# Optimization experiments

Measured on AMD Instinct MI355X. Metric: run time of the kernel, lower is better.

Reference implementation:

```python
import jax, jax.numpy as jnp
import numpy as np

B, H, W = 8, 1024, 1280
EPS = 1e-7
MIN_DEPTH, MAX_DEPTH = 10.0, 255.0


def _constants(batch, view_to_syn='left'):
    trans = np.array([-4.14339018, -0.0238197036, -0.00190685259], np.float32)
    K_u = np.array([1035.30811, 0.0, 596.955017, 0.0, 1035.08765, 520.410034, 0.0, 0.0, 1.0], np.float32).reshape(3, 3)
    K_u[0, :] /= 1280.0
    K_u[1, :] /= 1024.0
    K_u4 = np.zeros((4, 4), np.float32); K_u4[:3, :3] = K_u; K_u4[3, 3] = 1.0
    K_d = np.array([1035.17419, 0.0, 688.361877, 0.0, 1034.979, 521.070801, 0.0, 0.0, 1.0], np.float32).reshape(3, 3)
    K_d[0, :] /= 1280.0
    K_d[1, :] /= 1024.0
    K_d4 = np.zeros((4, 4), np.float32); K_d4[:3, :3] = K_d; K_d4[3, 3] = 1.0
    if view_to_syn == 'right':
        src, tgt, t = K_u4, K_d4, trans
    else:
        src, tgt, t = K_d4, K_u4, -trans
    source_K = jnp.asarray(np.tile(src[None], (batch, 1, 1)))
    target_K = jnp.asarray(np.tile(tgt[None], (batch, 1, 1)))
    trans_vec = jnp.asarray(np.tile(t[None], (batch, 1)))
    return source_K, target_K, trans_vec


def setup_inputs() -> dict:
    key = jax.random.key(0)
    k1, k2 = jax.random.split(key)
    img = jax.random.normal(k1, (B, 3, H, W), jnp.float32)
    pred_disp = jax.random.uniform(k2, (B, 1, H, W), jnp.float32)
    source_K, target_K, trans_vec = _constants(B, 'left')
    return {"img": img, "pred_disp": pred_disp, "source_K": source_K,
            "target_K": target_K, "trans_vec": trans_vec}


def _grid_sample_border(img, grid):
    """Bilinear grid_sample, padding_mode='border', align_corners=False (torch default).
    img: [B,C,H,W], grid: [B,H,W,2] in [-1,1] (x,y). Returns [B,C,H,W]."""
    b, c, h, w = img.shape
    x = (grid[..., 0] + 1.0) * w * 0.5 - 0.5  # [B,H,W]
    y = (grid[..., 1] + 1.0) * h * 0.5 - 0.5
    x0f = jnp.floor(x); y0f = jnp.floor(y)
    wx = (x - x0f)[:, None]  # [B,1,H,W]
    wy = (y - y0f)[:, None]
    x0 = jnp.clip(x0f.astype(jnp.int32), 0, w - 1)
    x1 = jnp.clip(x0f.astype(jnp.int32) + 1, 0, w - 1)
    y0 = jnp.clip(y0f.astype(jnp.int32), 0, h - 1)
    y1 = jnp.clip(y0f.astype(jnp.int32) + 1, 0, h - 1)
    gather = jax.vmap(lambda im, yi, xi: im[:, yi, xi])  # -> [B,C,H,W]
    i00 = gather(img, y0, x0)
    i01 = gather(img, y0, x1)
    i10 = gather(img, y1, x0)
    i11 = gather(img, y1, x1)
    return (i00 * (1 - wx) * (1 - wy) + i01 * wx * (1 - wy)
            + i10 * (1 - wx) * wy + i11 * wx * wy)


def reference(img, pred_disp, source_K, target_K, trans_vec):
    b, _, h, w = img.shape
    # disp -> depth
    min_disp, max_disp = 1.0 / MAX_DEPTH, 1.0 / MIN_DEPTH
    scaled_disp = min_disp + (max_disp - min_disp) * pred_disp
    depth = 1.0 / scaled_disp  # [B,1,H,W]
    # homogeneous pixel grid [3, H*W]
    xs, ys = jnp.meshgrid(jnp.arange(w, dtype=jnp.float32),
                          jnp.arange(h, dtype=jnp.float32), indexing='xy')
    pix = jnp.stack([xs.reshape(-1), ys.reshape(-1), jnp.ones(h * w, jnp.float32)], 0)
    # backproject
    inv_K = jnp.linalg.inv(source_K)[:, :3, :3]  # [B,3,3]
    cam = jnp.einsum('bij,jn->bin', inv_K, pix) * depth.reshape(b, 1, -1)  # [B,3,HW]
    cam4 = jnp.concatenate([cam, jnp.ones((b, 1, h * w), cam.dtype)], axis=1)  # [B,4,HW]
    # extrinsic: R = I, so T @ R = translation matrix
    T = jnp.tile(jnp.eye(4, dtype=img.dtype)[None], (b, 1, 1)).at[:, :3, 3].set(trans_vec.reshape(b, 3))
    P = jnp.matmul(target_K, T)[:, :3, :]  # [B,3,4]
    cp = jnp.matmul(P, cam4)  # [B,3,HW]
    pc = cp[:, :2] / (cp[:, 2:3] + EPS)  # [B,2,HW]
    pc = pc.reshape(b, 2, h, w).transpose(0, 2, 3, 1)  # [B,H,W,2]
    scale = jnp.array([w - 1, h - 1], dtype=pc.dtype)
    grid = (pc / scale - 0.5) * 2.0
    return _grid_sample_border(img, grid)
```

## Files before the change

### kernel.cpp

```cpp
#include <hip/hip_runtime.h>

#define BB 8
#define HH 1024
#define WW 1280
#define HW (HH * WW)
#define EPSF 1e-7f

#define TH 16
#define TCOLS 264
#define SROWS 18
#define CPR 66
#define CCH (SROWS * CPR)
#define CPT 5
#define STF (CPT * 256 * 4)

#define GAS __attribute__((address_space(1)))
#define LAS __attribute__((address_space(3)))

typedef float f4 __attribute__((ext_vector_type(4)));

__device__ __forceinline__ float fast_rcp(float x) {
    float r = __builtin_amdgcn_rcpf(x);
    r = r * __builtin_fmaf(-x, r, 2.0f);
    return r;
}

__global__ void precompute_consts(
    const float* __restrict__ srcK, const float* __restrict__ tgtK,
    const float* __restrict__ trans, float* __restrict__ cb)
{
    const int b = threadIdx.x;
    if (b >= BB) return;
    const float* sK = srcK + b * 16;
    const float* tK = tgtK + b * 16;
    const float* tv = trans + b * 3;

    const float fsx = sK[0], csx = sK[2];
    const float fsy = sK[5], csy = sK[6];
    const float ftx = tK[0], ctx = tK[2];
    const float fty = tK[5], cty = tK[6];
    const float t0 = tv[0], t1 = tv[1], t2 = tv[2];

    const float Sx = (float)WW / (float)(WW - 1);
    const float Sy = (float)HH / (float)(HH - 1);
    const float rfsx = 1.0f / fsx;
    const float rfsy = 1.0f / fsy;
    float* c = cb + b * 8;
    c[0] = ftx * rfsx * Sx;
    c[1] = __builtin_fmaf(-ftx * csx, rfsx, ctx) * Sx;
    c[2] = (ftx * t0 + ctx * t2) * Sx;
    c[3] = fty * rfsy * Sy;
    c[4] = __builtin_fmaf(-fty * csy, rfsy, cty) * Sy;
    c[5] = (fty * t1 + cty * t2) * Sy;
    c[6] = t2 + EPSF;
    c[7] = 0.0f;
}

__global__ __launch_bounds__(256, 4) void synth_view_kernel(
    const float* __restrict__ img, const float* __restrict__ disp,
    const float* __restrict__ cbuf, float* __restrict__ out)
{
    __shared__ __align__(16) float st[STF];

    const int tid = threadIdx.x;
    const int wid = blockIdx.x;
    const int r   = wid & 7;
    int q = wid >> 3;
    const int tyl = q & 7;  q >>= 3;
    const int xb  = q % 5;
    const int b   = q / 5;
    const int y0  = (r * 8 + tyl) * TH;
    const int x0  = xb * 256;
    const int x   = x0 + tid;

    const float* imb = img + (size_t)b * 3 * HW;

    const float* db = disp + (size_t)b * HW + (size_t)y0 * WW + x;
    float dsp[TH];
#pragma unroll
    for (int j = 0; j < TH; ++j)
        dsp[j] = __builtin_nontemporal_load(db + j * WW);

    int goff[CPT];
#pragma unroll
    for (int i = 0; i < CPT; ++i) {
        const int qq = i * 256 + tid;
        const int qc = min(qq, CCH - 1);
        const int ri = qc / CPR;
        const int k  = qc - ri * CPR;
        const int row = min(max(y0 - 1 + ri, 0), HH - 1);
        const int col = min(max(x0 - 4 + 4 * k, 0), WW - 4);
        goff[i] = row * WW + col;
    }

#pragma unroll
    for (int i = 0; i < CPT; ++i)
        __builtin_amdgcn_global_load_lds(
            (const GAS unsigned int*)(const void*)(imb + goff[i]),
            (LAS unsigned int*)(void*)&st[(i * 256 + tid) * 4], 16, 0, 0);

    const float* cb = cbuf + b * 8;
    const float A00 = cb[0], A02 = cb[1], C0 = cb[2];
    const float A11 = cb[3], A12 = cb[4], C1 = cb[5];
    const float t2e = cb[6];

    const float mind = 1.0f / 255.0f;
    const float rng  = 0.1f - mind;
    const float axc  = __builtin_fmaf(A00, (float)x, A02);

    int   lb[TH]; float wxa[TH], wya[TH];
#pragma unroll
    for (int j = 0; j < TH; ++j) {
        const int y = y0 + j;
        const float sd  = __builtin_fmaf(dsp[j], rng, mind);
        const float rrz = fast_rcp(__builtin_fmaf(t2e, sd, 1.0f));
        const float ayc = __builtin_fmaf(A11, (float)y, A12);
        const float sx  = __builtin_fmaf(__builtin_fmaf(C0, sd, axc), rrz, -0.5f);
        const float sy  = __builtin_fmaf(__builtin_fmaf(C1, sd, ayc), rrz, -0.5f);

        const int ixc = min(max((int)floorf(sx), 0), WW - 2);
        const int iyc = min(max((int)floorf(sy), 0), HH - 2);
        wxa[j] = fminf(fmaxf(sx - (float)ixc, 0.0f), 1.0f);
        wya[j] = fminf(fmaxf(sy - (float)iyc, 0.0f), 1.0f);
        const int wcol = min(max(ixc - x0 + 4, 0), TCOLS - 2);
        const int wrow = min(max(iyc - y0 + 1, 0), SROWS - 2);
        lb[j] = (wrow * TCOLS + wcol) * 4;
    }

    float* outb = out + (size_t)b * 3 * HW + (size_t)y0 * WW + x;

    for (int c = 0; c < 3; ++c) {
        if (c > 0) {
            __syncthreads();
#pragma unroll
            for (int i = 0; i < CPT; ++i)
                __builtin_amdgcn_global_load_lds(
                    (const GAS unsigned int*)(const void*)(imb + (size_t)c * HW + goff[i]),
                    (LAS unsigned int*)(void*)&st[(i * 256 + tid) * 4], 16, 0, 0);
        }
        __syncthreads();

        float* oc = outb + (size_t)c * HW;
#pragma unroll
        for (int j = 0; j < TH; ++j) {
            const float* p = (const float*)((const char*)st + lb[j]);
            const float wx = wxa[j], wy = wya[j];
            const float wxm = 1.0f - wx, wym = 1.0f - wy;
            float acc =          p[0]         * (wxm * wym);
            acc = __builtin_fmaf(p[1],         wx * wym, acc);
            acc = __builtin_fmaf(p[TCOLS],     wxm * wy, acc);
            acc = __builtin_fmaf(p[TCOLS + 1], wx * wy,  acc);
            __builtin_nontemporal_store(acc, oc + j * WW);
        }
    }
}

extern "C" void kernel_launch(void* const* d_in, const int* in_sizes, int n_in,
                              void* d_out, int out_size, void* d_ws, size_t ws_size,
                              hipStream_t stream) {
    const float* img   = (const float*)d_in[0];
    const float* disp  = (const float*)d_in[1];
    const float* srcK  = (const float*)d_in[2];
    const float* tgtK  = (const float*)d_in[3];
    const float* trans = (const float*)d_in[4];
    float* out = (float*)d_out;
    float* cb  = (float*)d_ws;

    precompute_consts<<<dim3(1), dim3(64), 0, stream>>>(srcK, tgtK, trans, cb);

    dim3 block(256, 1, 1);
    dim3 grid(5 * 64 * BB, 1, 1);
    synth_view_kernel<<<grid, block, 0, stream>>>(img, disp, cb, out);
}
```

Before: 253.9 us.

## Split channels across separate blocks instead of looping per block

Each block now handles one color channel, so the grid is three times larger and the serial per-channel loop with its extra barriers and LDS reloads is gone. The disparity load switches from nontemporal to a normal cached load, since each disparity tile is now read by three blocks. This adds parallelism and removes the intra-block channel serialization, at the cost of recomputing the projection coordinates three times and reading disparity three times.

New measurement: 256.1 us. About the same (+0.9%).

```diff
diff --git a/kernel.cpp b/kernel.cpp
--- a/kernel.cpp
+++ b/kernel.cpp
@@ -16,8 +16,6 @@
 
 #define GAS __attribute__((address_space(1)))
 #define LAS __attribute__((address_space(3)))
-
-typedef float f4 __attribute__((ext_vector_type(4)));
 
 __device__ __forceinline__ float fast_rcp(float x) {
     float r = __builtin_amdgcn_rcpf(x);
@@ -64,8 +62,10 @@
 
     const int tid = threadIdx.x;
     const int wid = blockIdx.x;
-    const int r   = wid & 7;
-    int q = wid >> 3;
+    const int c   = wid / 2560;
+    const int t   = wid - c * 2560;
+    const int r   = t & 7;
+    int q = t >> 3;
     const int tyl = q & 7;  q >>= 3;
     const int xb  = q % 5;
     const int b   = q / 5;
@@ -73,15 +73,14 @@
     const int x0  = xb * 256;
     const int x   = x0 + tid;
 
-    const float* imb = img + (size_t)b * 3 * HW;
+    const float* imc = img + ((size_t)b * 3 + c) * HW;
 
     const float* db = disp + (size_t)b * HW + (size_t)y0 * WW + x;
     float dsp[TH];
 #pragma unroll
     for (int j = 0; j < TH; ++j)
-        dsp[j] = __builtin_nontemporal_load(db + j * WW);
+        dsp[j] = db[j * WW];
 
-    int goff[CPT];
 #pragma unroll
     for (int i = 0; i < CPT; ++i) {
         const int qq = i * 256 + tid;
@@ -90,14 +89,10 @@
         const int k  = qc - ri * CPR;
         const int row = min(max(y0 - 1 + ri, 0), HH - 1);
         const int col = min(max(x0 - 4 + 4 * k, 0), WW - 4);
-        goff[i] = row * WW + col;
+        __builtin_amdgcn_global_load_lds(
+            (const GAS unsigned int*)(const void*)(imc + row * WW + col),
+            (LAS unsigned int*)(void*)&st[qq * 4], 16, 0, 0);
     }
-
-#pragma unroll
-    for (int i = 0; i < CPT; ++i)
-        __builtin_amdgcn_global_load_lds(
-            (const GAS unsigned int*)(const void*)(imb + goff[i]),
-            (LAS unsigned int*)(void*)&st[(i * 256 + tid) * 4], 16, 0, 0);
 
     const float* cb = cbuf + b * 8;
     const float A00 = cb[0], A02 = cb[1], C0 = cb[2];
@@ -127,31 +122,19 @@
         lb[j] = (wrow * TCOLS + wcol) * 4;
     }
 
-    float* outb = out + (size_t)b * 3 * HW + (size_t)y0 * WW + x;
+    __syncthreads();
 
-    for (int c = 0; c < 3; ++c) {
-        if (c > 0) {
-            __syncthreads();
+    float* oc = out + ((size_t)b * 3 + c) * HW + (size_t)y0 * WW + x;
 #pragma unroll
-            for (int i = 0; i < CPT; ++i)
-                __builtin_amdgcn_global_load_lds(
-                    (const GAS unsigned int*)(const void*)(imb + (size_t)c * HW + goff[i]),
-                    (LAS unsigned int*)(void*)&st[(i * 256 + tid) * 4], 16, 0, 0);
-        }
-        __syncthreads();
-
-        float* oc = outb + (size_t)c * HW;
-#pragma unroll
-        for (int j = 0; j < TH; ++j) {
-            const float* p = (const float*)((const char*)st + lb[j]);
-            const float wx = wxa[j], wy = wya[j];
-            const float wxm = 1.0f - wx, wym = 1.0f - wy;
-            float acc =          p[0]         * (wxm * wym);
-            acc = __builtin_fmaf(p[1],         wx * wym, acc);
-            acc = __builtin_fmaf(p[TCOLS],     wxm * wy, acc);
-            acc = __builtin_fmaf(p[TCOLS + 1], wx * wy,  acc);
-            __builtin_nontemporal_store(acc, oc + j * WW);
-        }
+    for (int j = 0; j < TH; ++j) {
+        const float* p = (const float*)((const char*)st + lb[j]);
+        const float wx = wxa[j], wy = wya[j];
+        const float wxm = 1.0f - wx, wym = 1.0f - wy;
+        float acc =          p[0]         * (wxm * wym);
+        acc = __builtin_fmaf(p[1],         wx * wym, acc);
+        acc = __builtin_fmaf(p[TCOLS],     wxm * wy, acc);
+        acc = __builtin_fmaf(p[TCOLS + 1], wx * wy,  acc);
+        __builtin_nontemporal_store(acc, oc + j * WW);
     }
 }
 
@@ -169,6 +152,6 @@
     precompute_consts<<<dim3(1), dim3(64), 0, stream>>>(srcK, tgtK, trans, cb);
 
     dim3 block(256, 1, 1);
-    dim3 grid(5 * 64 * BB, 1, 1);
+    dim3 grid(3 * 5 * 64 * BB, 1, 1);
     synth_view_kernel<<<grid, block, 0, stream>>>(img, disp, cb, out);
 }
```
